# Optimization experiments

Measured on AMD Instinct MI355X. Metric: run time of the kernel, lower is better.

## Reference

```python
import jax, jax.numpy as jnp
import numpy as np

DIM = 512
CHUNK = 64
LN_EPS = 1e-5


def setup_inputs() -> dict:
    key = jax.random.key(0)
    ks = jax.random.split(key, 9)
    B, S, D = 4, 4096, DIM
    x = jax.random.normal(ks[0], (B, S, D), dtype=jnp.float32)
    # Linear weights stored as [in, out] (equivalent to torch W.T)
    W_omega = jax.random.normal(ks[1], (D, D), dtype=jnp.float32) / np.sqrt(D)
    b_omega = jnp.zeros((D,), dtype=jnp.float32)
    log_scale = jnp.full((D,), np.log(0.1), dtype=jnp.float32)
    ln_gamma = jnp.ones((4 * D,), dtype=jnp.float32)
    ln_beta = jnp.zeros((4 * D,), dtype=jnp.float32)
    W1 = jax.random.normal(ks[2], (4 * D, 2 * D), dtype=jnp.float32) / np.sqrt(4 * D)
    b1 = jnp.zeros((2 * D,), dtype=jnp.float32)
    W2 = jax.random.normal(ks[3], (2 * D, D), dtype=jnp.float32) / np.sqrt(2 * D)
    b2 = jnp.zeros((D,), dtype=jnp.float32)
    return {"x": x, "W_omega": W_omega, "b_omega": b_omega, "log_scale": log_scale,
            "ln_gamma": ln_gamma, "ln_beta": ln_beta, "W1": W1, "b1": b1, "W2": W2, "b2": b2}


def reference(x, W_omega, b_omega, log_scale, ln_gamma, ln_beta, W1, b1, W2, b2):
    B, S, D = x.shape
    C = CHUNK
    # S chosen as multiple of C, so pad_len == 0 (matches torch no-pad branch)
    N = S // C
    omega = x @ W_omega + b_omega                      # [B,S,D]
    oc = omega.reshape(B, N, C, D)
    xc = x.reshape(B, N, C, D)
    pos = jnp.arange(1, C + 1, dtype=x.dtype)          # [C]
    pos_scale = (1.0 / jnp.sqrt(pos))[None, None, :, None]
    scale = jnp.exp(log_scale)
    phi = jnp.cumsum(oc * scale * pos_scale, axis=2)   # [B,N,C,D]
    cos_phi = jnp.cos(phi)
    sin_phi = jnp.sin(phi)
    cr = xc * cos_phi                                   # content modulated real
    ci = xc * sin_phi                                   # content modulated imag
    pos_norm = pos[None, None, :, None]
    mr = jnp.cumsum(cr, axis=2) / pos_norm              # memory real
    mi = jnp.cumsum(ci, axis=2) / pos_norm              # memory imag
    rr = mr * cos_phi + mi * sin_phi                    # retrieved real
    ri = mi * cos_phi - mr * sin_phi                    # retrieved imag
    ctx = jnp.concatenate([cr.reshape(B, S, D), ci.reshape(B, S, D),
                           rr.reshape(B, S, D), ri.reshape(B, S, D)], axis=-1)  # [B,S,4D]
    mu = jnp.mean(ctx, axis=-1, keepdims=True)
    var = jnp.mean((ctx - mu) ** 2, axis=-1, keepdims=True)
    h = (ctx - mu) / jnp.sqrt(var + LN_EPS) * ln_gamma + ln_beta
    h = h @ W1 + b1
    h = jax.nn.gelu(h, approximate=False)               # torch GELU default = exact erf
    out = h @ W2 + b2                                   # dropout is identity at eval
    return x + out
```

## Files before the change

### kernel.cpp

```cpp
#include <hip/hip_runtime.h>
#include <hip/hip_bf16.h>
#include <math.h>


typedef __bf16 bf16x8 __attribute__((ext_vector_type(8)));
typedef __bf16 bf16x4 __attribute__((ext_vector_type(4)));
typedef __bf16 bf16x2 __attribute__((ext_vector_type(2)));
typedef float  f32x4  __attribute__((ext_vector_type(4)));

typedef __attribute__((address_space(1))) void* gas_ptr;
typedef __attribute__((address_space(3))) void* las_ptr;

__device__ __forceinline__ void load_lds16(const void* g, void* l) {
    __builtin_amdgcn_global_load_lds((gas_ptr)g, (las_ptr)l, 16, 0, 0);
}

__global__ void cast_kernel(const float* __restrict__ in, __bf16* __restrict__ out, int n4)
{
    int i = blockIdx.x * blockDim.x + threadIdx.x;
    if (i < n4) {
        float4 v = ((const float4*)in)[i];
        bf16x4 o = { (__bf16)v.x, (__bf16)v.y, (__bf16)v.z, (__bf16)v.w };
        ((bf16x4*)out)[i] = o;
    }
}

__global__ void transpose_cast_kernel(const float* __restrict__ in, __bf16* __restrict__ out,
                                      int K, int N)
{
    __shared__ float tile[32][33];
    int n0 = blockIdx.x * 32, k0 = blockIdx.y * 32;
    int tx = threadIdx.x, ty = threadIdx.y;
    #pragma unroll
    for (int i = 0; i < 32; i += 8)
        tile[ty + i][tx] = in[(size_t)(k0 + ty + i) * N + n0 + tx];
    __syncthreads();
    #pragma unroll
    for (int i = 0; i < 32; i += 8)
        out[(size_t)(n0 + ty + i) * K + k0 + tx] = (__bf16)tile[tx][ty + i];
}

template<int MODE>
__global__ __launch_bounds__(256)
void gemm_kernel(const __bf16* __restrict__ A, const __bf16* __restrict__ Bt,
                 const float* __restrict__ bias, const float* __restrict__ resid,
                 void* __restrict__ out, int M, int N, int K)
{
    __shared__ __bf16 As[128 * 64];
    __shared__ __bf16 Bs[128 * 64];

    const int tid     = threadIdx.x;
    const int tiles_n = N >> 7;
    const int ln_tn   = __ffs(tiles_n) - 1;
    const int per_m   = (M >> 7) >> 3;

    const int xcd = blockIdx.x & 7;
    const int j   = blockIdx.x >> 3;
    const int tile_m = (xcd * per_m + (j >> ln_tn)) << 7;
    const int tile_n = (j & (tiles_n - 1)) << 7;

    const int wave = tid >> 6;
    const int lane = tid & 63;

    const int srow = lane >> 3;
    const int scol = ((lane & 7) ^ srow) << 3;

    const __bf16* Ags = A  + (size_t)(tile_m + wave * 32 + srow) * K + scol;
    const __bf16* Bgs = Bt + (size_t)(tile_n + wave * 32 + srow) * K + scol;

    const int m0 = (wave >> 1) << 6;
    const int n0 = (wave & 1) << 6;
    const int lr = lane & 15;
    const int q  = lane >> 4;
    const int l7 = lane & 7;
    const int fc0 = ((0 + q) ^ l7) << 3;
    const int fc1 = ((4 + q) ^ l7) << 3;

    f32x4 acc[4][4];
    #pragma unroll
    for (int i = 0; i < 4; ++i)
        #pragma unroll
        for (int jj = 0; jj < 4; ++jj)
            acc[i][jj] = (f32x4){0.f, 0.f, 0.f, 0.f};

    for (int k0 = 0; k0 < K; k0 += 64) {
        __syncthreads();
        #pragma unroll
        for (int c = 0; c < 4; ++c) {
            load_lds16(Ags + k0 + (size_t)(c * 8) * K, &As[(wave * 32 + c * 8) * 64]);
            load_lds16(Bgs + k0 + (size_t)(c * 8) * K, &Bs[(wave * 32 + c * 8) * 64]);
        }
        __syncthreads();

        {
            bf16x8 af[4], bq[4];
            #pragma unroll
            for (int i = 0; i < 4; ++i)
                af[i] = *(const bf16x8*)&As[(m0 + i * 16 + lr) * 64 + fc0];
            #pragma unroll
            for (int jj = 0; jj < 4; ++jj)
                bq[jj] = *(const bf16x8*)&Bs[(n0 + jj * 16 + lr) * 64 + fc0];
            #pragma unroll
            for (int i = 0; i < 4; ++i)
                #pragma unroll
                for (int jj = 0; jj < 4; ++jj)
                    acc[i][jj] = __builtin_amdgcn_mfma_f32_16x16x32_bf16(af[i], bq[jj], acc[i][jj], 0, 0, 0);
        }
        {
            bf16x8 af[4], bq[4];
            #pragma unroll
            for (int i = 0; i < 4; ++i)
                af[i] = *(const bf16x8*)&As[(m0 + i * 16 + lr) * 64 + fc1];
            #pragma unroll
            for (int jj = 0; jj < 4; ++jj)
                bq[jj] = *(const bf16x8*)&Bs[(n0 + jj * 16 + lr) * 64 + fc1];
            #pragma unroll
            for (int i = 0; i < 4; ++i)
                #pragma unroll
                for (int jj = 0; jj < 4; ++jj)
                    acc[i][jj] = __builtin_amdgcn_mfma_f32_16x16x32_bf16(af[i], bq[jj], acc[i][jj], 0, 0, 0);
        }
    }

    const int orow0 = tile_m + m0 + (q << 2);
    const int ocol0 = tile_n + n0 + lr;
    #pragma unroll
    for (int i = 0; i < 4; ++i) {
        #pragma unroll
        for (int jj = 0; jj < 4; ++jj) {
            const int col = ocol0 + jj * 16;
            const float bv = bias[col];
            #pragma unroll
            for (int r = 0; r < 4; ++r) {
                const int row = orow0 + i * 16 + r;
                float v = acc[i][jj][r] + bv;
                size_t idx = (size_t)row * N + col;
                if (MODE == 0) {
                    ((float*)out)[idx] = v;
                } else if (MODE == 1) {
                    float g = 0.5f * v * (1.0f + erff(v * 0.70710678118654752f));
                    ((__bf16*)out)[idx] = (__bf16)g;
                } else {
                    ((float*)out)[idx] = v + resid[idx];
                }
            }
        }
    }
}

__global__ __launch_bounds__(256)
void scan_ln_kernel(const float* __restrict__ x, const float* __restrict__ omega,
                    const float* __restrict__ log_scale,
                    const float* __restrict__ gamma, const float* __restrict__ beta,
                    __bf16* __restrict__ ctx)
{
    const int chunk = blockIdx.x;
    const int t     = threadIdx.x;
    const int d     = t << 1;
    const int lane  = t & 63, wv = t >> 6;
    const size_t base = (size_t)chunk * 64 * 512;

    const float2 ls = *(const float2*)&log_scale[d];
    const float sc0 = expf(ls.x), sc1 = expf(ls.y);
    const float2 ga = *(const float2*)&gamma[d];
    const float2 gb = *(const float2*)&gamma[512 + d];
    const float2 gc = *(const float2*)&gamma[1024 + d];
    const float2 gd = *(const float2*)&gamma[1536 + d];
    const float2 ba = *(const float2*)&beta[d];
    const float2 bb = *(const float2*)&beta[512 + d];
    const float2 bc = *(const float2*)&beta[1024 + d];
    const float2 bd = *(const float2*)&beta[1536 + d];

    float ph0 = 0.f, ph1 = 0.f;
    float sr0 = 0.f, si0 = 0.f, sr1 = 0.f, si1 = 0.f;
    __shared__ float red[2][8];

    float2 om_n = *(const float2*)&omega[base + d];
    float2 xv_n = *(const float2*)&x[base + d];

    for (int c = 0; c < 64; ++c) {
        const float2 om = om_n;
        const float2 xv = xv_n;
        if (c < 63) {
            om_n = *(const float2*)&omega[base + (size_t)(c + 1) * 512 + d];
            xv_n = *(const float2*)&x[base + (size_t)(c + 1) * 512 + d];
        }
        const float psc = rsqrtf((float)(c + 1));
        ph0 += om.x * sc0 * psc;
        ph1 += om.y * sc1 * psc;
        float sp0, cp0, sp1, cp1;
        __sincosf(ph0, &sp0, &cp0);
        __sincosf(ph1, &sp1, &cp1);
        const float cr0 = xv.x * cp0, ci0 = xv.x * sp0;
        const float cr1 = xv.y * cp1, ci1 = xv.y * sp1;
        sr0 += cr0; si0 += ci0; sr1 += cr1; si1 += ci1;
        const float inv = 1.0f / (float)(c + 1);
        const float mr0 = sr0 * inv, mi0 = si0 * inv;
        const float mr1 = sr1 * inv, mi1 = si1 * inv;
        const float rr0 = mr0 * cp0 + mi0 * sp0;
        const float ri0 = mi0 * cp0 - mr0 * sp0;
        const float rr1 = mr1 * cp1 + mi1 * sp1;
        const float ri1 = mi1 * cp1 - mr1 * sp1;

        float s  = cr0 + ci0 + rr0 + ri0 + cr1 + ci1 + rr1 + ri1;
        float s2 = cr0*cr0 + ci0*ci0 + rr0*rr0 + ri0*ri0
                 + cr1*cr1 + ci1*ci1 + rr1*rr1 + ri1*ri1;
        #pragma unroll
        for (int o = 32; o > 0; o >>= 1) {
            s  += __shfl_down(s, o);
            s2 += __shfl_down(s2, o);
        }
        if (lane == 0) { red[c & 1][wv] = s; red[c & 1][4 + wv] = s2; }
        __syncthreads();
        const float S  = red[c & 1][0] + red[c & 1][1] + red[c & 1][2] + red[c & 1][3];
        const float S2 = red[c & 1][4] + red[c & 1][5] + red[c & 1][6] + red[c & 1][7];
        const float mu   = S * (1.0f / 2048.0f);
        const float var  = S2 * (1.0f / 2048.0f) - mu * mu;
        const float rstd = rsqrtf(var + 1e-5f);

        const size_t ob = ((size_t)chunk * 64 + c) * 2048;
        *(bf16x2*)&ctx[ob + d] =
            (bf16x2){ (__bf16)(((cr0 - mu) * rstd) * ga.x + ba.x),
                      (__bf16)(((cr1 - mu) * rstd) * ga.y + ba.y) };
        *(bf16x2*)&ctx[ob + 512 + d] =
            (bf16x2){ (__bf16)(((ci0 - mu) * rstd) * gb.x + bb.x),
                      (__bf16)(((ci1 - mu) * rstd) * gb.y + bb.y) };
        *(bf16x2*)&ctx[ob + 1024 + d] =
            (bf16x2){ (__bf16)(((rr0 - mu) * rstd) * gc.x + bc.x),
                      (__bf16)(((rr1 - mu) * rstd) * gc.y + bc.y) };
        *(bf16x2*)&ctx[ob + 1536 + d] =
            (bf16x2){ (__bf16)(((ri0 - mu) * rstd) * gd.x + bd.x),
                      (__bf16)(((ri1 - mu) * rstd) * gd.y + bd.y) };
    }
}

extern "C" void kernel_launch(void* const* d_in, const int* in_sizes, int n_in,
                              void* d_out, int out_size, void* d_ws, size_t ws_size,
                              hipStream_t stream)
{
    const float* x         = (const float*)d_in[0];
    const float* W_omega   = (const float*)d_in[1];
    const float* b_omega   = (const float*)d_in[2];
    const float* log_scale = (const float*)d_in[3];
    const float* ln_gamma  = (const float*)d_in[4];
    const float* ln_beta   = (const float*)d_in[5];
    const float* W1        = (const float*)d_in[6];
    const float* b1        = (const float*)d_in[7];
    const float* W2        = (const float*)d_in[8];
    const float* b2        = (const float*)d_in[9];
    float* out = (float*)d_out;

    char* ws = (char*)d_ws;
    __bf16* xb    = (__bf16*)(ws);
    __bf16* womT  = (__bf16*)(ws + 16777216);
    __bf16* w1T   = (__bf16*)(ws + 17301504);
    __bf16* w2T   = (__bf16*)(ws + 21495808);
    float*  omega = (float*) (ws + 22544384);
    __bf16* hbuf  = (__bf16*)(ws + 22544384);
    __bf16* ctx   = (__bf16*)(ws + 56098816);

    cast_kernel<<<8192, 256, 0, stream>>>(x, xb, 2097152);
    transpose_cast_kernel<<<dim3(16, 16), dim3(32, 8), 0, stream>>>(W_omega, womT, 512, 512);
    transpose_cast_kernel<<<dim3(32, 64), dim3(32, 8), 0, stream>>>(W1,      w1T,  2048, 1024);
    transpose_cast_kernel<<<dim3(16, 32), dim3(32, 8), 0, stream>>>(W2,      w2T,  1024, 512);

    gemm_kernel<0><<<512, 256, 0, stream>>>(xb, womT, b_omega, nullptr, omega, 16384, 512, 512);

    scan_ln_kernel<<<256, 256, 0, stream>>>(x, omega, log_scale, ln_gamma, ln_beta, ctx);

    gemm_kernel<1><<<1024, 256, 0, stream>>>(ctx, w1T, b1, nullptr, hbuf, 16384, 1024, 2048);

    gemm_kernel<2><<<512, 256, 0, stream>>>(hbuf, w2T, b2, x, out, 16384, 512, 1024);
}
```

Measured before the change: 297.2 us.

## Double-buffer GEMM LDS tiles, store omega in bf16, widen scan kernel

The GEMM main loop now uses two LDS buffers. The next K-tile's async global-to-LDS loads are issued before computing on the current tile, and one of the two barriers per iteration is removed, so load latency can overlap with MFMA work. The omega projection is written as bf16 instead of fp32, and the scan/LayerNorm kernel reads the bf16 omega and bf16 x, which halves the traffic of that intermediate at some cost in phase precision. The scan kernel moves to 512 threads with one feature per thread for more parallelism per chunk. The extra LDS per block may lower occupancy, and the bf16 phase inputs add rounding error to the sin/cos arguments.

Measured after the change: 283.2 us. 4.7% less time.

```diff
diff --git a/kernel.cpp b/kernel.cpp
--- a/kernel.cpp
+++ b/kernel.cpp
@@ -46,8 +46,8 @@
                  const float* __restrict__ bias, const float* __restrict__ resid,
                  void* __restrict__ out, int M, int N, int K)
 {
-    __shared__ __bf16 As[128 * 64];
-    __shared__ __bf16 Bs[128 * 64];
+    __shared__ __bf16 As[2][128 * 64];
+    __shared__ __bf16 Bs[2][128 * 64];
 
     const int tid     = threadIdx.x;
     const int tiles_n = N >> 7;
@@ -83,23 +83,36 @@
         for (int jj = 0; jj < 4; ++jj)
             acc[i][jj] = (f32x4){0.f, 0.f, 0.f, 0.f};
 
-    for (int k0 = 0; k0 < K; k0 += 64) {
+    const int nIter = K >> 6;
+
+    #pragma unroll
+    for (int c = 0; c < 4; ++c) {
+        load_lds16(Ags + (size_t)(c * 8) * K, &As[0][(wave * 32 + c * 8) * 64]);
+        load_lds16(Bgs + (size_t)(c * 8) * K, &Bs[0][(wave * 32 + c * 8) * 64]);
+    }
+
+    for (int it = 0; it < nIter; ++it) {
+        const int cur = it & 1;
         __syncthreads();
-        #pragma unroll
-        for (int c = 0; c < 4; ++c) {
-            load_lds16(Ags + k0 + (size_t)(c * 8) * K, &As[(wave * 32 + c * 8) * 64]);
-            load_lds16(Bgs + k0 + (size_t)(c * 8) * K, &Bs[(wave * 32 + c * 8) * 64]);
-        }
-        __syncthreads();
-
+        if (it + 1 < nIter) {
+            const int nk = (it + 1) << 6;
+            #pragma unroll
+            for (int c = 0; c < 4; ++c) {
+                load_lds16(Ags + nk + (size_t)(c * 8) * K, &As[cur ^ 1][(wave * 32 + c * 8) * 64]);
+                load_lds16(Bgs + nk + (size_t)(c * 8) * K, &Bs[cur ^ 1][(wave * 32 + c * 8) * 64]);
+            }
+        }
+
+        const __bf16* as = As[cur];
+        const __bf16* bs = Bs[cur];
         {
             bf16x8 af[4], bq[4];
             #pragma unroll
             for (int i = 0; i < 4; ++i)
-                af[i] = *(const bf16x8*)&As[(m0 + i * 16 + lr) * 64 + fc0];
+                af[i] = *(const bf16x8*)&as[(m0 + i * 16 + lr) * 64 + fc0];
             #pragma unroll
             for (int jj = 0; jj < 4; ++jj)
-                bq[jj] = *(const bf16x8*)&Bs[(n0 + jj * 16 + lr) * 64 + fc0];
+                bq[jj] = *(const bf16x8*)&bs[(n0 + jj * 16 + lr) * 64 + fc0];
             #pragma unroll
             for (int i = 0; i < 4; ++i)
                 #pragma unroll
@@ -110,10 +123,10 @@
             bf16x8 af[4], bq[4];
             #pragma unroll
             for (int i = 0; i < 4; ++i)
-                af[i] = *(const bf16x8*)&As[(m0 + i * 16 + lr) * 64 + fc1];
+                af[i] = *(const bf16x8*)&as[(m0 + i * 16 + lr) * 64 + fc1];
             #pragma unroll
             for (int jj = 0; jj < 4; ++jj)
-                bq[jj] = *(const bf16x8*)&Bs[(n0 + jj * 16 + lr) * 64 + fc1];
+                bq[jj] = *(const bf16x8*)&bs[(n0 + jj * 16 + lr) * 64 + fc1];
             #pragma unroll
             for (int i = 0; i < 4; ++i)
                 #pragma unroll
@@ -136,7 +149,7 @@
                 float v = acc[i][jj][r] + bv;
                 size_t idx = (size_t)row * N + col;
                 if (MODE == 0) {
-                    ((float*)out)[idx] = v;
+                    ((__bf16*)out)[idx] = (__bf16)v;
                 } else if (MODE == 1) {
                     float g = 0.5f * v * (1.0f + erff(v * 0.70710678118654752f));
                     ((__bf16*)out)[idx] = (__bf16)g;
@@ -148,89 +161,65 @@
     }
 }
 
-__global__ __launch_bounds__(256)
-void scan_ln_kernel(const float* __restrict__ x, const float* __restrict__ omega,
+__global__ __launch_bounds__(512)
+void scan_ln_kernel(const __bf16* __restrict__ xb, const __bf16* __restrict__ omega,
                     const float* __restrict__ log_scale,
                     const float* __restrict__ gamma, const float* __restrict__ beta,
                     __bf16* __restrict__ ctx)
 {
     const int chunk = blockIdx.x;
-    const int t     = threadIdx.x;
-    const int d     = t << 1;
-    const int lane  = t & 63, wv = t >> 6;
+    const int d     = threadIdx.x;
+    const int lane  = d & 63, wv = d >> 6;
     const size_t base = (size_t)chunk * 64 * 512;
 
-    const float2 ls = *(const float2*)&log_scale[d];
-    const float sc0 = expf(ls.x), sc1 = expf(ls.y);
-    const float2 ga = *(const float2*)&gamma[d];
-    const float2 gb = *(const float2*)&gamma[512 + d];
-    const float2 gc = *(const float2*)&gamma[1024 + d];
-    const float2 gd = *(const float2*)&gamma[1536 + d];
-    const float2 ba = *(const float2*)&beta[d];
-    const float2 bb = *(const float2*)&beta[512 + d];
-    const float2 bc = *(const float2*)&beta[1024 + d];
-    const float2 bd = *(const float2*)&beta[1536 + d];
-
-    float ph0 = 0.f, ph1 = 0.f;
-    float sr0 = 0.f, si0 = 0.f, sr1 = 0.f, si1 = 0.f;
-    __shared__ float red[2][8];
-
-    float2 om_n = *(const float2*)&omega[base + d];
-    float2 xv_n = *(const float2*)&x[base + d];
+    const float scale = expf(log_scale[d]);
+    const float g0 = gamma[d], g1 = gamma[512 + d], g2 = gamma[1024 + d], g3 = gamma[1536 + d];
+    const float e0 = beta[d],  e1 = beta[512 + d],  e2 = beta[1024 + d],  e3 = beta[1536 + d];
+
+    float phi = 0.f, scr = 0.f, sci = 0.f;
+    __shared__ float red[2][16];
+
+    float om_n = (float)omega[base + d];
+    float xv_n = (float)xb[base + d];
 
     for (int c = 0; c < 64; ++c) {
-        const float2 om = om_n;
-        const float2 xv = xv_n;
+        const float om = om_n;
+        const float xv = xv_n;
         if (c < 63) {
-            om_n = *(const float2*)&omega[base + (size_t)(c + 1) * 512 + d];
-            xv_n = *(const float2*)&x[base + (size_t)(c + 1) * 512 + d];
-        }
-        const float psc = rsqrtf((float)(c + 1));
-        ph0 += om.x * sc0 * psc;
-        ph1 += om.y * sc1 * psc;
-        float sp0, cp0, sp1, cp1;
-        __sincosf(ph0, &sp0, &cp0);
-        __sincosf(ph1, &sp1, &cp1);
-        const float cr0 = xv.x * cp0, ci0 = xv.x * sp0;
-        const float cr1 = xv.y * cp1, ci1 = xv.y * sp1;
-        sr0 += cr0; si0 += ci0; sr1 += cr1; si1 += ci1;
+            om_n = (float)omega[base + (size_t)(c + 1) * 512 + d];
+            xv_n = (float)xb[base + (size_t)(c + 1) * 512 + d];
+        }
+        phi += om * scale * rsqrtf((float)(c + 1));
+        float sp, cp;
+        __sincosf(phi, &sp, &cp);
+        const float cr = xv * cp, ci = xv * sp;
+        scr += cr; sci += ci;
         const float inv = 1.0f / (float)(c + 1);
-        const float mr0 = sr0 * inv, mi0 = si0 * inv;
-        const float mr1 = sr1 * inv, mi1 = si1 * inv;
-        const float rr0 = mr0 * cp0 + mi0 * sp0;
-        const float ri0 = mi0 * cp0 - mr0 * sp0;
-        const float rr1 = mr1 * cp1 + mi1 * sp1;
-        const float ri1 = mi1 * cp1 - mr1 * sp1;
-
-        float s  = cr0 + ci0 + rr0 + ri0 + cr1 + ci1 + rr1 + ri1;
-        float s2 = cr0*cr0 + ci0*ci0 + rr0*rr0 + ri0*ri0
-                 + cr1*cr1 + ci1*ci1 + rr1*rr1 + ri1*ri1;
+        const float mr = scr * inv, mi = sci * inv;
+        const float rr = mr * cp + mi * sp;
+        const float ri = mi * cp - mr * sp;
+
+        float s  = cr + ci + rr + ri;
+        float s2 = cr * cr + ci * ci + rr * rr + ri * ri;
         #pragma unroll
         for (int o = 32; o > 0; o >>= 1) {
             s  += __shfl_down(s, o);
             s2 += __shfl_down(s2, o);
         }
-        if (lane == 0) { red[c & 1][wv] = s; red[c & 1][4 + wv] = s2; }
+        if (lane == 0) { red[c & 1][wv] = s; red[c & 1][8 + wv] = s2; }
         __syncthreads();
-        const float S  = red[c & 1][0] + red[c & 1][1] + red[c & 1][2] + red[c & 1][3];
-        const float S2 = red[c & 1][4] + red[c & 1][5] + red[c & 1][6] + red[c & 1][7];
+        float S = 0.f, S2 = 0.f;
+        #pragma unroll
+        for (int i = 0; i < 8; ++i) { S += red[c & 1][i]; S2 += red[c & 1][8 + i]; }
         const float mu   = S * (1.0f / 2048.0f);
         const float var  = S2 * (1.0f / 2048.0f) - mu * mu;
         const float rstd = rsqrtf(var + 1e-5f);
 
         const size_t ob = ((size_t)chunk * 64 + c) * 2048;
-        *(bf16x2*)&ctx[ob + d] =
-            (bf16x2){ (__bf16)(((cr0 - mu) * rstd) * ga.x + ba.x),
-                      (__bf16)(((cr1 - mu) * rstd) * ga.y + ba.y) };
-        *(bf16x2*)&ctx[ob + 512 + d] =
-            (bf16x2){ (__bf16)(((ci0 - mu) * rstd) * gb.x + bb.x),
-                      (__bf16)(((ci1 - mu) * rstd) * gb.y + bb.y) };
-        *(bf16x2*)&ctx[ob + 1024 + d] =
-            (bf16x2){ (__bf16)(((rr0 - mu) * rstd) * gc.x + bc.x),
-                      (__bf16)(((rr1 - mu) * rstd) * gc.y + bc.y) };
-        *(bf16x2*)&ctx[ob + 1536 + d] =
-            (bf16x2){ (__bf16)(((ri0 - mu) * rstd) * gd.x + bd.x),
-                      (__bf16)(((ri1 - mu) * rstd) * gd.y + bd.y) };
+        ctx[ob + d]        = (__bf16)(((cr - mu) * rstd) * g0 + e0);
+        ctx[ob + 512 + d]  = (__bf16)(((ci - mu) * rstd) * g1 + e1);
+        ctx[ob + 1024 + d] = (__bf16)(((rr - mu) * rstd) * g2 + e2);
+        ctx[ob + 1536 + d] = (__bf16)(((ri - mu) * rstd) * g3 + e3);
     }
 }
 
@@ -255,7 +244,7 @@
     __bf16* womT  = (__bf16*)(ws + 16777216);
     __bf16* w1T   = (__bf16*)(ws + 17301504);
     __bf16* w2T   = (__bf16*)(ws + 21495808);
-    float*  omega = (float*) (ws + 22544384);
+    __bf16* omega = (__bf16*)(ws + 22544384);
     __bf16* hbuf  = (__bf16*)(ws + 22544384);
     __bf16* ctx   = (__bf16*)(ws + 56098816);
 
@@ -266,7 +255,7 @@
 
     gemm_kernel<0><<<512, 256, 0, stream>>>(xb, womT, b_omega, nullptr, omega, 16384, 512, 512);
 
-    scan_ln_kernel<<<256, 256, 0, stream>>>(x, omega, log_scale, ln_gamma, ln_beta, ctx);
+    scan_ln_kernel<<<256, 512, 0, stream>>>(xb, omega, log_scale, ln_gamma, ln_beta, ctx);
 
     gemm_kernel<1><<<1024, 256, 0, stream>>>(ctx, w1T, b1, nullptr, hbuf, 16384, 1024, 2048);
 
```
